# Performance work log

Hardware: AMD Instinct MI355X
Metric: run time of the kernel (lower is better)

The kernel has to match this reference:

```python
import jax, jax.numpy as jnp
import numpy as np

B, CI, CO, K, SD, H, W = 8, 128, 128, 3, 512, 256, 256


def setup_inputs() -> dict:
    key = jax.random.key(0)
    k0, k1, k2, k3 = jax.random.split(key, 4)
    x = jax.random.normal(k0, (B, CI, H, W), jnp.float32)
    style = jax.random.normal(k1, (B, SD), jnp.float32)
    # learned params
    w_base = jax.random.normal(k2, (1, CO, CI, K, K), jnp.float32)   # ModulatedConv2d.weight
    aff_w = jax.random.normal(k3, (CI, SD), jnp.float32)             # affine weight [out=CI, in=SD]
    aff_b = jnp.ones((CI,), jnp.float32)                             # bias_init=1
    return {"x": x, "style": style, "w_base": w_base, "aff_w": aff_w, "aff_b": aff_b}


def reference(x, style, w_base, aff_w, aff_b):
    b, ci, h, w_ = x.shape
    co, k = w_base.shape[1], w_base.shape[3]
    # affine: FullyConnectedLayer, linear activation, weight_gain = 1/sqrt(style_dim)
    aff_gain = 1.0 / np.sqrt(aff_w.shape[1])
    s = style @ (aff_w * aff_gain).T + aff_b                 # [B, CI]
    # modulate
    wgain = 1.0 / np.sqrt(ci * k * k)
    wt = w_base * wgain * s[:, None, :, None, None]          # [B, CO, CI, K, K]
    # demodulate
    d = jax.lax.rsqrt(jnp.sum(wt * wt, axis=(2, 3, 4)) + 1e-8)  # [B, CO]
    wt = wt * d[:, :, None, None, None]
    # grouped conv, groups = batch, padding = k//2 (up=down=1 path)
    wt = wt.reshape(b * co, ci, k, k)
    xg = x.reshape(1, b * ci, h, w_)
    pad = k // 2
    y = jax.lax.conv_general_dilated(
        xg, wt, window_strides=(1, 1), padding=[(pad, pad), (pad, pad)],
        dimension_numbers=("NCHW", "OIHW", "NCHW"), feature_group_count=b)
    return y.reshape(b, co, h, w_)
```

## Files before the change

### kernel.cpp

```cpp
#include <hip/hip_runtime.h>
#include <stdint.h>

#define BB 8
#define SD 512

typedef unsigned short u16;
typedef __attribute__((ext_vector_type(8))) __bf16 bf16x8;
typedef __attribute__((ext_vector_type(16))) float f32x16;

__device__ float g_s[BB * 128];
__device__ u16 g_wtb[BB * 9 * 2 * 8192];
__device__ u16 g_xb[(size_t)BB * 258 * 258 * 128 + 2048];

typedef const __attribute__((address_space(1))) uint32_t* gp1;
typedef __attribute__((address_space(3))) uint32_t* lp3;

__device__ __forceinline__ void glds16(const void* g, void* l) {
    __builtin_amdgcn_global_load_lds((gp1)g, (lp3)l, 16, 0, 0);
}
__device__ __forceinline__ void glds4(const void* g, void* l) {
    __builtin_amdgcn_global_load_lds((gp1)g, (lp3)l, 4, 0, 0);
}

__device__ __forceinline__ u16 f2bf(float f) {
    uint32_t u = __float_as_uint(f);
    u += 0x7FFFu + ((u >> 16) & 1u);
    return (u16)(u >> 16);
}

__global__ void affine_kernel(const float* __restrict__ style,
                              const float* __restrict__ aff_w,
                              const float* __restrict__ aff_b) {
    int b = blockIdx.x;
    int ci = threadIdx.x;
    const float gain = 0.044194173824159216f;
    const float* st = style + b * SD;
    const float* aw = aff_w + ci * SD;
    float acc = 0.f;
    #pragma unroll 8
    for (int j = 0; j < SD; ++j) acc += st[j] * aw[j];
    g_s[b * 128 + ci] = acc * gain + aff_b[ci];
}

__global__ __launch_bounds__(256) void modulate_kernel(const float* __restrict__ w_base) {
    int blk = blockIdx.x;
    int b = blk >> 7, co = blk & 127;
    int tid = threadIdx.x;
    const float wgain = 0.029462782549439483f;
    const int n = 1152;
    const float* wb = w_base + co * n;
    const float* sp = g_s + b * 128;

    float v[5];
    float sq = 0.f;
    #pragma unroll
    for (int i = 0; i < 5; ++i) {
        int idx = tid + i * 256;
        float w = 0.f;
        if (idx < n) {
            int ci = idx / 9;
            w = wb[idx] * wgain * sp[ci];
        }
        v[i] = w;
        sq += w * w;
    }
    #pragma unroll
    for (int off = 32; off > 0; off >>= 1) sq += __shfl_down(sq, off, 64);
    __shared__ float red[4];
    int lane = tid & 63, wvi = tid >> 6;
    if (lane == 0) red[wvi] = sq;
    __syncthreads();
    float tot = red[0] + red[1] + red[2] + red[3];
    float d = rsqrtf(tot + 1e-8f);
    #pragma unroll
    for (int i = 0; i < 5; ++i) {
        int idx = tid + i * 256;
        if (idx < n) {
            int ci = idx / 9;
            int k9 = idx - ci * 9;
            u16 hv = f2bf(v[i] * d);
            int ci64 = ci & 63;
            size_t base = ((size_t)(b * 9 + k9) * 2 + (ci >> 6)) * 8192;
            g_wtb[base + co * 64 + (ci64 ^ ((co & 7) << 3))] = hv;
        }
    }
}

__global__ __launch_bounds__(256) void zero_border_kernel() {
    int b = blockIdx.x;
    uint4 z = make_uint4(0, 0, 0, 0);
    char* xbB = (char*)g_xb;
    for (int i = threadIdx.x; i < 16448; i += 256) {
        size_t pix; int k;
        if (i < 4128)       { pix = (size_t)(b * 258 + 0)   * 258 + (i >> 4);            k = i & 15; }
        else if (i < 8256)  { int j = i - 4128;  pix = (size_t)(b * 258 + 257) * 258 + (j >> 4);       k = j & 15; }
        else if (i < 12352) { int j = i - 8256;  pix = (size_t)(b * 258 + 1 + (j >> 4)) * 258 + 0;     k = j & 15; }
        else                { int j = i - 12352; pix = (size_t)(b * 258 + 1 + (j >> 4)) * 258 + 257;   k = j & 15; }
        *(uint4*)(xbB + pix * 256 + (size_t)k * 16) = z;
    }
}

__global__ __launch_bounds__(256) void transpose_kernel(const float* __restrict__ x) {
    __shared__ __align__(16) u16 t_lds[64 * 128];
    const int chunk = blockIdx.x;
    const int gy = blockIdx.y;
    const int b = blockIdx.z;
    const int px0 = chunk * 64;
    const int tid = threadIdx.x;
    const int pq = tid & 15;
    const int cig = tid >> 4;

    const float* base = x + (size_t)b * 128 * 65536 + (size_t)gy * 256 + px0 + pq * 4;
    char* ldsB = (char*)t_lds;

    float4 v[8];
    #pragma unroll
    for (int c = 0; c < 8; ++c)
        v[c] = *(const float4*)(base + (size_t)(cig * 8 + c) * 65536);

    #pragma unroll
    for (int j = 0; j < 4; ++j) {
        uint32_t dw[4];
        #pragma unroll
        for (int d = 0; d < 4; ++d) {
            const float* lo4 = (const float*)&v[2 * d];
            const float* hi4 = (const float*)&v[2 * d + 1];
            dw[d] = (uint32_t)f2bf(lo4[j]) | ((uint32_t)f2bf(hi4[j]) << 16);
        }
        int px = pq * 4 + j;
        int key = (px0 + px + 1) & 7;
        int slot = cig ^ key;
        *(uint4*)(ldsB + px * 256 + slot * 16) = *(uint4*)dw;
    }
    __syncthreads();

    char* outB = (char*)g_xb;
    #pragma unroll
    for (int it = 0; it < 4; ++it) {
        int flat = it * 256 + tid;
        int r = flat >> 4, k = flat & 15;
        size_t pix = ((size_t)(b * 258 + gy + 1)) * 258 + (px0 + r + 1);
        *(uint4*)(outB + pix * 256 + k * 16) = *(const uint4*)(ldsB + r * 256 + k * 16);
    }
}

__global__ __launch_bounds__(512, 4) void conv_kernel(float* __restrict__ y) {
    __shared__ __align__(16) u16 xs[10 * 34 * 64];
    __shared__ __align__(16) u16 ab[2][8192];

    const int b = blockIdx.y;
    const int t = blockIdx.x;
    const int swzt = (t & 7) * 32 + (t >> 3);
    const int tx = swzt & 7, ty = swzt >> 3;
    const int y0 = ty * 8, x0 = tx * 32;
    const int tid = threadIdx.x;
    const int lane = tid & 63, wv = tid >> 6;
    const int l31 = lane & 31;
    const int l5 = lane >> 5;
    const int coHalf = (wv & 1) * 64;
    const int py0w = (wv >> 1) * 2;

    const char* xbB = (const char*)g_xb;
    const char* wtbB = (const char*)(g_wtb) + (size_t)b * 294912;
    char* xsB = (char*)xs;

    f32x16 acc[2][2];
    #pragma unroll
    for (int mf = 0; mf < 2; ++mf)
        #pragma unroll
        for (int rf = 0; rf < 2; ++rf)
            acc[mf][rf] = (f32x16){0.f};

    for (int h = 0; h < 2; ++h) {
        for (int i = wv; i < 50; i += 8) {
            int row = i / 5, sub = i - row * 5;
            size_t pixb = ((size_t)(b * 258 + y0 + row) * 258 + x0) * 256 + h * 128;
            char* dst = xsB + row * 4352;
            if (sub < 4) {
                glds16(xbB + pixb + (size_t)(sub * 8 + (lane >> 3)) * 256 + (lane & 7) * 16,
                       dst + sub * 1024);
            } else {
                glds4(xbB + pixb + (size_t)(32 + (lane >> 5)) * 256 + (lane & 31) * 4,
                      dst + 4096);
            }
        }
        if (h == 0) {
            #pragma unroll
            for (int q = 0; q < 2; ++q) {
                int j = wv * 2 + q;
                glds16(wtbB + j * 1024 + lane * 16, (char*)ab[0] + j * 1024);
            }
        }
        __syncthreads();

        for (int tap = 0; tap < 9; ++tap) {
            int s = h * 9 + tap;
            if (s < 17) {
                int ns = s + 1;
                int ntap = (ns >= 9) ? (ns - 9) : ns;
                int nh = (ns >= 9) ? 1 : h;
                const char* src = wtbB + (ntap * 2 + nh) * 16384;
                char* dst = (char*)ab[ns & 1];
                #pragma unroll
                for (int q = 0; q < 2; ++q) {
                    int j = wv * 2 + q;
                    glds16(src + j * 1024 + lane * 16, dst + j * 1024);
                }
            }

            const int ky = tap / 3, kx = tap - ky * 3;
            const char* abuf = (const char*)ab[s & 1];
            const int bcol = l31 + kx;
            const int bkey = bcol & 7;
            const int brow_base = (py0w + ky) * 34 + bcol;

            #pragma unroll
            for (int ks = 0; ks < 4; ++ks) {
                const int cig = ks * 2 + l5;
                bf16x8 af[2];
                #pragma unroll
                for (int mf = 0; mf < 2; ++mf) {
                    int co = coHalf + mf * 32 + l31;
                    af[mf] = *(const bf16x8*)(abuf + co * 128 + ((cig ^ (co & 7)) << 4));
                }
                bf16x8 bf[2];
                #pragma unroll
                for (int rf = 0; rf < 2; ++rf)
                    bf[rf] = *(const bf16x8*)(xsB + (brow_base + rf * 34) * 128 +
                                              ((cig ^ bkey) << 4));
                __builtin_amdgcn_s_setprio(1);
                #pragma unroll
                for (int mf = 0; mf < 2; ++mf)
                    #pragma unroll
                    for (int rf = 0; rf < 2; ++rf)
                        acc[mf][rf] = __builtin_amdgcn_mfma_f32_32x32x16_bf16(
                            af[mf], bf[rf], acc[mf][rf], 0, 0, 0);
                __builtin_amdgcn_s_setprio(0);
            }
            __syncthreads();
        }
    }

    float* yb = y + (size_t)b * 128 * 65536;
    #pragma unroll
    for (int mf = 0; mf < 2; ++mf) {
        #pragma unroll
        for (int rf = 0; rf < 2; ++rf) {
            int gy = y0 + py0w + rf;
            int gx = x0 + l31;
            #pragma unroll
            for (int j = 0; j < 16; ++j) {
                int co = coHalf + mf * 32 + (j & 3) + 8 * (j >> 2) + 4 * l5;
                yb[(size_t)co * 65536 + gy * 256 + gx] = acc[mf][rf][j];
            }
        }
    }
}

extern "C" void kernel_launch(void* const* d_in, const int* in_sizes, int n_in,
                              void* d_out, int out_size, void* d_ws, size_t ws_size,
                              hipStream_t stream) {
    const float* x = (const float*)d_in[0];
    const float* style = (const float*)d_in[1];
    const float* w_base = (const float*)d_in[2];
    const float* aff_w = (const float*)d_in[3];
    const float* aff_b = (const float*)d_in[4];
    float* y = (float*)d_out;

    affine_kernel<<<BB, 128, 0, stream>>>(style, aff_w, aff_b);
    modulate_kernel<<<BB * 128, 256, 0, stream>>>(w_base);
    zero_border_kernel<<<BB, 256, 0, stream>>>();
    transpose_kernel<<<dim3(4, 256, BB), 256, 0, stream>>>(x);
    conv_kernel<<<dim3(256, BB), 512, 0, stream>>>(y);
}
```

Baseline: 326.6 us.

## Switch to channel-slot-major layouts for padded input and weights

The padded bf16 input buffer is reorganised from pixel-major with 128 interleaved channels into 16 planes of 8-channel slots, and the weights into slot-major blocks. The conv kernel's LDS tile and fragment reads now use these contiguous slot planes without XOR swizzling, and the transpose and border-zero kernels write the new layout. This is meant to simplify address math and make per-lane fragment reads contiguous. In exchange, global loads into LDS are now 16-byte entries gathered from scattered rows and planes, which may cost coalescing, and the unswizzled LDS strides may introduce bank conflicts.

```diff
diff --git a/kernel.cpp b/kernel.cpp
--- a/kernel.cpp
+++ b/kernel.cpp
@@ -3,6 +3,7 @@
 
 #define BB 8
 #define SD 512
+#define PP 66564
 
 typedef unsigned short u16;
 typedef __attribute__((ext_vector_type(8))) __bf16 bf16x8;
@@ -79,9 +80,9 @@
             int ci = idx / 9;
             int k9 = idx - ci * 9;
             u16 hv = f2bf(v[i] * d);
-            int ci64 = ci & 63;
+            int slot = (ci & 63) >> 3, e = ci & 7;
             size_t base = ((size_t)(b * 9 + k9) * 2 + (ci >> 6)) * 8192;
-            g_wtb[base + co * 64 + (ci64 ^ ((co & 7) << 3))] = hv;
+            g_wtb[base + slot * 1024 + co * 8 + e] = hv;
         }
     }
 }
@@ -91,12 +92,14 @@
     uint4 z = make_uint4(0, 0, 0, 0);
     char* xbB = (char*)g_xb;
     for (int i = threadIdx.x; i < 16448; i += 256) {
-        size_t pix; int k;
-        if (i < 4128)       { pix = (size_t)(b * 258 + 0)   * 258 + (i >> 4);            k = i & 15; }
-        else if (i < 8256)  { int j = i - 4128;  pix = (size_t)(b * 258 + 257) * 258 + (j >> 4);       k = j & 15; }
-        else if (i < 12352) { int j = i - 8256;  pix = (size_t)(b * 258 + 1 + (j >> 4)) * 258 + 0;     k = j & 15; }
-        else                { int j = i - 12352; pix = (size_t)(b * 258 + 1 + (j >> 4)) * 258 + 257;   k = j & 15; }
-        *(uint4*)(xbB + pix * 256 + (size_t)k * 16) = z;
+        int plane = i / 1028, rem = i - plane * 1028;
+        int gy, gx;
+        if (rem < 258)      { gy = 0;             gx = rem; }
+        else if (rem < 516) { gy = 257;           gx = rem - 258; }
+        else if (rem < 772) { gy = rem - 516 + 1; gx = 0; }
+        else                { gy = rem - 772 + 1; gx = 257; }
+        size_t a16 = (size_t)(b * 16 + plane) * PP + (size_t)gy * 258 + gx;
+        *(uint4*)(xbB + a16 * 16) = z;
     }
 }
 
@@ -139,13 +142,15 @@
     for (int it = 0; it < 4; ++it) {
         int flat = it * 256 + tid;
         int r = flat >> 4, k = flat & 15;
-        size_t pix = ((size_t)(b * 258 + gy + 1)) * 258 + (px0 + r + 1);
-        *(uint4*)(outB + pix * 256 + k * 16) = *(const uint4*)(ldsB + r * 256 + k * 16);
+        int key = (px0 + r + 1) & 7;
+        uint4 val = *(const uint4*)(ldsB + r * 256 + ((k ^ key) << 4));
+        size_t a16 = (size_t)(b * 16 + k) * PP + (size_t)(gy + 1) * 258 + (px0 + r + 1);
+        *(uint4*)(outB + a16 * 16) = val;
     }
 }
 
 __global__ __launch_bounds__(512, 4) void conv_kernel(float* __restrict__ y) {
-    __shared__ __align__(16) u16 xs[10 * 34 * 64];
+    __shared__ __align__(16) u16 xs[2720 * 8];
     __shared__ __align__(16) u16 ab[2][8192];
 
     const int b = blockIdx.y;
@@ -172,16 +177,25 @@
             acc[mf][rf] = (f32x16){0.f};
 
     for (int h = 0; h < 2; ++h) {
-        for (int i = wv; i < 50; i += 8) {
-            int row = i / 5, sub = i - row * 5;
-            size_t pixb = ((size_t)(b * 258 + y0 + row) * 258 + x0) * 256 + h * 128;
-            char* dst = xsB + row * 4352;
-            if (sub < 4) {
-                glds16(xbB + pixb + (size_t)(sub * 8 + (lane >> 3)) * 256 + (lane & 7) * 16,
-                       dst + sub * 1024);
+        for (int i = wv; i < 44; i += 8) {
+            if (i < 42) {
+                int entry = i * 64 + lane;
+                int slot = entry / 340;
+                int rem = entry - slot * 340;
+                int row = rem / 34;
+                int col = rem - row * 34;
+                size_t a16 = (size_t)(b * 16 + h * 8 + slot) * PP +
+                             (size_t)(y0 + row) * 258 + (x0 + col);
+                glds16(xbB + a16 * 16, xsB + i * 1024);
             } else {
-                glds4(xbB + pixb + (size_t)(32 + (lane >> 5)) * 256 + (lane & 31) * 4,
-                      dst + 4096);
+                int j = i - 42;
+                int entry = 2688 + j * 16 + (lane >> 2);
+                int rem = entry - 2380;
+                int row = rem / 34;
+                int col = rem - row * 34;
+                size_t a16 = (size_t)(b * 16 + h * 8 + 7) * PP +
+                             (size_t)(y0 + row) * 258 + (x0 + col);
+                glds4(xbB + a16 * 16 + (lane & 3) * 4, xsB + 43008 + j * 256);
             }
         }
         if (h == 0) {
@@ -210,9 +224,7 @@
 
             const int ky = tap / 3, kx = tap - ky * 3;
             const char* abuf = (const char*)ab[s & 1];
-            const int bcol = l31 + kx;
-            const int bkey = bcol & 7;
-            const int brow_base = (py0w + ky) * 34 + bcol;
+            const int brow = (py0w + ky) * 34 + l31 + kx;
 
             #pragma unroll
             for (int ks = 0; ks < 4; ++ks) {
@@ -221,13 +233,12 @@
                 #pragma unroll
                 for (int mf = 0; mf < 2; ++mf) {
                     int co = coHalf + mf * 32 + l31;
-                    af[mf] = *(const bf16x8*)(abuf + co * 128 + ((cig ^ (co & 7)) << 4));
+                    af[mf] = *(const bf16x8*)(abuf + cig * 2048 + co * 16);
                 }
                 bf16x8 bf[2];
                 #pragma unroll
                 for (int rf = 0; rf < 2; ++rf)
-                    bf[rf] = *(const bf16x8*)(xsB + (brow_base + rf * 34) * 128 +
-                                              ((cig ^ bkey) << 4));
+                    bf[rf] = *(const bf16x8*)(xsB + (cig * 340 + brow + rf * 34) * 16);
                 __builtin_amdgcn_s_setprio(1);
                 #pragma unroll
                 for (int mf = 0; mf < 2; ++mf)
```

Result: slower. 389.5 us (+19.3%).
